# Optimization experiments

Hardware: AMD Instinct MI355X
Metric: run time of the kernel (lower is better)

## Reference

```python
import jax, jax.numpy as jnp
import numpy as np

N_ACTIONS = 4
R_DIM = 32
A_DIM = 32
FORGET = 0.05
Q_INIT = 0.0
B, T = 8192, 1024


def setup_inputs() -> dict:
    key = jax.random.key(0)
    ks = jax.random.split(key, 10)
    actions = jax.random.randint(ks[0], (B, T), 0, N_ACTIONS, dtype=jnp.int64 if jax.config.jax_enable_x64 else jnp.int32)
    rewards = jax.random.uniform(ks[1], (B, T), dtype=jnp.float32)
    s = 0.1
    w_r1 = jax.random.normal(ks[2], (R_DIM, 1 + R_DIM), dtype=jnp.float32) * s
    b_r1 = jax.random.normal(ks[3], (R_DIM,), dtype=jnp.float32) * s
    w_r2 = jax.random.normal(ks[4], (1, R_DIM), dtype=jnp.float32) * s
    b_r2 = jax.random.normal(ks[5], (1,), dtype=jnp.float32) * s
    w_a1 = jax.random.normal(ks[6], (A_DIM, N_ACTIONS + A_DIM), dtype=jnp.float32) * s
    b_a1 = jax.random.normal(ks[7], (A_DIM,), dtype=jnp.float32) * s
    w_a2 = jax.random.normal(ks[8], (N_ACTIONS, A_DIM), dtype=jnp.float32) * s
    b_a2 = jax.random.normal(ks[9], (N_ACTIONS,), dtype=jnp.float32) * s
    return {"actions": actions, "rewards": rewards,
            "w_r1": w_r1, "b_r1": b_r1, "w_r2": w_r2, "b_r2": b_r2,
            "w_a1": w_a1, "b_a1": b_a1, "w_a2": w_a2, "b_a2": b_a2}


def reference(actions, rewards, w_r1, b_r1, w_r2, b_r2, w_a1, b_a1, w_a2, b_a2):
    Bsz = actions.shape[0]
    q0 = jnp.full((Bsz, N_ACTIONS), Q_INIT, dtype=jnp.float32)
    sr0 = jnp.zeros((Bsz, R_DIM), dtype=jnp.float32)
    sa0 = jnp.zeros((Bsz, A_DIM), dtype=jnp.float32)

    def step(carry, xs):
        q, sr, sa = carry
        a_prev, r_prev = xs                        # [B] int, [B] float
        a_onehot = jax.nn.one_hot(a_prev, N_ACTIONS, dtype=jnp.float32)
        # reward module
        x_r = jnp.concatenate([r_prev[:, None], sr], axis=-1)   # [B, 1+R]
        sr_t = jnp.tanh(x_r @ w_r1.T + b_r1)                    # [B, R]
        q_new = sr_t @ w_r2.T + b_r2                            # [B, 1]
        # decay + chosen update
        q_decay = q + FORGET * (Q_INIT - q)
        q_t = q_decay * (1.0 - a_onehot) + q_new * a_onehot
        # action-history module
        x_a = jnp.concatenate([a_onehot, sa], axis=-1)          # [B, A+4]
        sa_t = jnp.tanh(x_a @ w_a1.T + b_a1)                    # [B, A]
        c_t = sa_t @ w_a2.T + b_a2                              # [B, 4]
        logits = q_t + c_t
        return (q_t, sr_t, sa_t), logits

    xs = (actions[:, :-1].T, rewards[:, :-1].T)   # time-major [T-1, B]
    _, logits_tm = jax.lax.scan(step, (q0, sr0, sa0), xs)
    return jnp.transpose(logits_tm, (1, 0, 2))    # [B, T-1, 4]
```

## Files before the change

kernel.cpp:

```cpp
#include <hip/hip_runtime.h>

#define TL 1024
#define NT 1023

typedef __bf16 bf16x8 __attribute__((ext_vector_type(8)));
typedef float  f32x4  __attribute__((ext_vector_type(4)));

__device__ __forceinline__ f32x4 mfma_bf16(bf16x8 a, bf16x8 b, f32x4 c) {
  return __builtin_amdgcn_mfma_f32_16x16x32_bf16(a, b, c, 0, 0, 0);
}

__device__ __forceinline__ unsigned pk_hi(unsigned e, unsigned o) {
  return __builtin_amdgcn_perm(o, e, 0x07060302u);
}

__device__ __forceinline__ float fast_tanh(float x) {
  float e = __builtin_amdgcn_exp2f(x * 2.8853900817779268f);
  float r = __builtin_amdgcn_rcpf(e + 1.0f);
  return fmaf(-2.0f, r, 1.0f);
}

__device__ __forceinline__ void split8(const float x[8], bf16x8& hi, bf16x8& lo) {
  unsigned h[4], l[4];
#pragma unroll
  for (int j = 0; j < 4; ++j) {
    unsigned eu = __float_as_uint(x[2 * j]);
    unsigned ou = __float_as_uint(x[2 * j + 1]);
    h[j] = pk_hi(eu, ou);
    float el = x[2 * j]     - __uint_as_float(eu & 0xFFFF0000u);
    float ol = x[2 * j + 1] - __uint_as_float(ou & 0xFFFF0000u);
    l[j] = pk_hi(__float_as_uint(el), __float_as_uint(ol));
  }
  hi = __builtin_bit_cast(bf16x8, make_uint4(h[0], h[1], h[2], h[3]));
  lo = __builtin_bit_cast(bf16x8, make_uint4(l[0], l[1], l[2], l[3]));
}

__global__ __launch_bounds__(128, 1) void memann_kernel(
    const int* __restrict__ actions, const float* __restrict__ rewards,
    const float* __restrict__ w_r1, const float* __restrict__ b_r1,
    const float* __restrict__ w_r2, const float* __restrict__ b_r2,
    const float* __restrict__ w_a1, const float* __restrict__ b_a1,
    const float* __restrict__ w_a2, const float* __restrict__ b_a2,
    float* __restrict__ out) {
  const int tid = threadIdx.x;
  const int wid = tid >> 6;
  const int l   = tid & 63;
  const int b0  = blockIdx.x * 16;
  const int m  = l & 15;
  const int ga = l >> 4;
  const int c  = l & 15;
  const int gD = l >> 4;

  __shared__ __align__(16) float tbl[2][4][64][4];
  __shared__ __align__(16) float csb[2][8][64];

  if (wid == 1) {
#pragma unroll
    for (int h = 0; h < 2; ++h)
#pragma unroll
      for (int a = 0; a < 4; ++a)
#pragma unroll
        for (int i = 0; i < 4; ++i) {
          const int row = 8 * gD + 4 * h + i;
          tbl[h][a][l][i] = b_a1[row] + w_a1[row * 36 + a];
        }
  }
  __syncthreads();

  const uint4 z4 = make_uint4(0u, 0u, 0u, 0u);
  const f32x4 zero = {0.f, 0.f, 0.f, 0.f};
  const int rowA = 8 * (m >> 2) + (m & 3);
  float wt[8];
  const int* arow = actions + (size_t)(b0 + c) * TL;

  if (wid == 0) {
    bf16x8 AWr_h[2], AWr_l[2], AQ_h, AQ_l;
#pragma unroll
    for (int h = 0; h < 2; ++h) {
#pragma unroll
      for (int i = 0; i < 8; ++i)
        wt[i] = w_r1[(rowA + 4 * h) * 33 + 1 + 8 * ga + i];
      split8(wt, AWr_h[h], AWr_l[h]);
    }
#pragma unroll
    for (int i = 0; i < 8; ++i) wt[i] = w_r2[8 * ga + i];
    split8(wt, AQ_h, AQ_l);

    float br1p[8], wr0p[8];
#pragma unroll
    for (int i = 0; i < 4; ++i) {
      br1p[i]     = b_r1[8 * gD + i];
      wr0p[i]     = w_r1[(8 * gD + i) * 33];
      br1p[4 + i] = b_r1[8 * gD + 4 + i];
      wr0p[4 + i] = w_r1[(8 * gD + 4 + i) * 33];
    }
    const float br2  = b_r2[0];
    const float ba2g = b_a2[gD];

    const float* rrow = rewards + (size_t)(b0 + c) * TL;
    float* outp = out + (size_t)(b0 + c) * NT * 4 + gD;

    int4   a_cur[2], a_nxt[2];
    float4 r_cur[2], r_nxt[2];
    a_cur[0] = *(const int4*)(arow);
    a_cur[1] = *(const int4*)(arow + 4);
    r_cur[0] = *(const float4*)(rrow);
    r_cur[1] = *(const float4*)(rrow + 4);
    a_nxt[0] = *(const int4*)(arow + 8);
    a_nxt[1] = *(const int4*)(arow + 12);
    r_nxt[0] = *(const float4*)(rrow + 8);
    r_nxt[1] = *(const float4*)(rrow + 12);

    bf16x8 Bh = __builtin_bit_cast(bf16x8, z4), Bl = Bh;
    float qv = 0.0f;
    float qreg[8];

    for (int cI = 0; cI < 128; ++cI) {
#pragma unroll
      for (int j = 0; j < 8; ++j) {
        const int4   av = a_cur[j >> 2];
        const float4 rv = r_cur[j >> 2];
        const int   a  = ((j & 3) == 0) ? av.x : ((j & 3) == 1) ? av.y
                        : ((j & 3) == 2) ? av.z : av.w;
        const float rc = ((j & 3) == 0) ? rv.x : ((j & 3) == 1) ? rv.y
                        : ((j & 3) == 2) ? rv.z : rv.w;

        f32x4 cR0, cR1;
#pragma unroll
        for (int i = 0; i < 4; ++i) {
          cR0[i] = fmaf(wr0p[i],     rc, br1p[i]);
          cR1[i] = fmaf(wr0p[4 + i], rc, br1p[4 + i]);
        }

        f32x4 dR0 = mfma_bf16(AWr_h[0], Bh, cR0);
        f32x4 dR1 = mfma_bf16(AWr_h[1], Bh, cR1);
        dR0 = mfma_bf16(AWr_h[0], Bl, dR0);
        dR1 = mfma_bf16(AWr_h[1], Bl, dR1);
        dR0 = mfma_bf16(AWr_l[0], Bh, dR0);
        dR1 = mfma_bf16(AWr_l[1], Bh, dR1);

        float xr[8];
#pragma unroll
        for (int i = 0; i < 4; ++i) {
          xr[i]     = fast_tanh(dR0[i]);
          xr[4 + i] = fast_tanh(dR1[i]);
        }
        split8(xr, Bh, Bl);

        f32x4 dq = mfma_bf16(AQ_h, Bh, zero);
        dq = mfma_bf16(AQ_h, Bl, dq);
        dq = mfma_bf16(AQ_l, Bh, dq);

        const float qn = dq[0] + br2;
        qv = (a == gD) ? qn : qv * 0.95f;
        qreg[j] = qv;
      }

      __syncthreads();

      const float* cb = &csb[cI & 1][0][0];
#pragma unroll
      for (int j = 0; j < 8; ++j) {
        const int t = 8 * cI + j;
        if (t < NT) outp[(size_t)t * 4] = (qreg[j] + cb[j * 64 + l]) + ba2g;
      }

      a_cur[0] = a_nxt[0];  a_cur[1] = a_nxt[1];
      r_cur[0] = r_nxt[0];  r_cur[1] = r_nxt[1];
      int tp = 8 * cI + 16;
      if (tp > TL - 8) tp = TL - 8;
      a_nxt[0] = *(const int4*)(arow + tp);
      a_nxt[1] = *(const int4*)(arow + tp + 4);
      r_nxt[0] = *(const float4*)(rrow + tp);
      r_nxt[1] = *(const float4*)(rrow + tp + 4);
    }
  } else {
    bf16x8 AWa_h[2], AWa_l[2], AC_h, AC_l;
#pragma unroll
    for (int h = 0; h < 2; ++h) {
#pragma unroll
      for (int i = 0; i < 8; ++i)
        wt[i] = w_a1[(rowA + 4 * h) * 36 + 4 + 8 * ga + i];
      split8(wt, AWa_h[h], AWa_l[h]);
    }
#pragma unroll
    for (int i = 0; i < 8; ++i) wt[i] = w_a2[(m & 3) * 32 + 8 * ga + i];
    split8(wt, AC_h, AC_l);

    int4 a_cur[2], a_nxt[2];
    a_cur[0] = *(const int4*)(arow);
    a_cur[1] = *(const int4*)(arow + 4);
    a_nxt[0] = *(const int4*)(arow + 8);
    a_nxt[1] = *(const int4*)(arow + 12);

    bf16x8 Bh = __builtin_bit_cast(bf16x8, z4), Bl = Bh;

    for (int cI = 0; cI < 128; ++cI) {
      float* cb = &csb[cI & 1][0][0];
#pragma unroll
      for (int j = 0; j < 8; ++j) {
        const int4 av = a_cur[j >> 2];
        const int  a  = ((j & 3) == 0) ? av.x : ((j & 3) == 1) ? av.y
                       : ((j & 3) == 2) ? av.z : av.w;

        const f32x4 pa0 = *(const f32x4*)&tbl[0][a][l][0];
        const f32x4 pa1 = *(const f32x4*)&tbl[1][a][l][0];

        f32x4 dA0 = mfma_bf16(AWa_h[0], Bh, zero);
        f32x4 dA1 = mfma_bf16(AWa_h[1], Bh, zero);
        dA0 = mfma_bf16(AWa_h[0], Bl, dA0);
        dA1 = mfma_bf16(AWa_h[1], Bl, dA1);
        dA0 = mfma_bf16(AWa_l[0], Bh, dA0);
        dA1 = mfma_bf16(AWa_l[1], Bh, dA1);

        float xa[8];
#pragma unroll
        for (int i = 0; i < 4; ++i) {
          xa[i]     = fast_tanh(dA0[i] + pa0[i]);
          xa[4 + i] = fast_tanh(dA1[i] + pa1[i]);
        }
        split8(xa, Bh, Bl);

        f32x4 dc = mfma_bf16(AC_h, Bh, zero);
        dc = mfma_bf16(AC_h, Bl, dc);
        dc = mfma_bf16(AC_l, Bh, dc);

        const float cs = (gD & 2) ? ((gD & 1) ? dc[3] : dc[2])
                                  : ((gD & 1) ? dc[1] : dc[0]);
        cb[j * 64 + l] = cs;
      }

      __syncthreads();

      a_cur[0] = a_nxt[0];  a_cur[1] = a_nxt[1];
      int tp = 8 * cI + 16;
      if (tp > TL - 8) tp = TL - 8;
      a_nxt[0] = *(const int4*)(arow + tp);
      a_nxt[1] = *(const int4*)(arow + tp + 4);
    }
  }
}


extern "C" void kernel_launch(void* const* d_in, const int* in_sizes, int n_in,
                              void* d_out, int out_size, void* d_ws,
                              size_t ws_size, hipStream_t stream) {
  const int* actions = (const int*)d_in[0];
  const float* rewards = (const float*)d_in[1];
  const float* w_r1 = (const float*)d_in[2];
  const float* b_r1 = (const float*)d_in[3];
  const float* w_r2 = (const float*)d_in[4];
  const float* b_r2 = (const float*)d_in[5];
  const float* w_a1 = (const float*)d_in[6];
  const float* b_a1 = (const float*)d_in[7];
  const float* w_a2 = (const float*)d_in[8];
  const float* b_a2 = (const float*)d_in[9];
  float* out = (float*)d_out;

  const int B = in_sizes[0] / TL;
  const int blocks = B / 16;

  hipLaunchKernelGGL(memann_kernel, dim3(blocks), dim3(128), 0, stream,
                     actions, rewards, w_r1, b_r1, w_r2, b_r2, w_a1, b_a1,
                     w_a2, b_a2, out);
}
```

Measured before the change: 678.7 us.

## Interleave two independent batch groups per wave to hide recurrence latency

Each block now handles 32 batch rows instead of 16, and each wave runs two independent recurrences interleaved in software. While one group's MFMA chain is in flight, the other group's tanh, split and head MFMAs run, with sched_barrier fences keeping that order. The aim is to hide the serial MFMA-to-tanh dependency latency of the scan. The cost is half as many blocks (256 for this batch size), more registers per wave, and a one-step skew in output indexing that has to be handled correctly.

```diff
diff --git a/kernel.cpp b/kernel.cpp
--- a/kernel.cpp
+++ b/kernel.cpp
@@ -34,6 +34,63 @@
   hi = __builtin_bit_cast(bf16x8, make_uint4(h[0], h[1], h[2], h[3]));
   lo = __builtin_bit_cast(bf16x8, make_uint4(l[0], l[1], l[2], l[3]));
 }
+
+static __device__ __forceinline__ int exti(const int4 v[2], int j) {
+  const int4 w = v[j >> 2];
+  return (j & 3) == 0 ? w.x : (j & 3) == 1 ? w.y : (j & 3) == 2 ? w.z : w.w;
+}
+static __device__ __forceinline__ float extf(const float4 v[2], int j) {
+  const float4 w = v[j >> 2];
+  return (j & 3) == 0 ? w.x : (j & 3) == 1 ? w.y : (j & 3) == 2 ? w.z : w.w;
+}
+
+__device__ __forceinline__ void rec6(const bf16x8& Ah0, const bf16x8& Ah1,
+                                     const bf16x8& Al0, const bf16x8& Al1,
+                                     const bf16x8& Bh, const bf16x8& Bl,
+                                     const f32x4& c0, const f32x4& c1,
+                                     f32x4& o0, f32x4& o1) {
+  f32x4 d0 = mfma_bf16(Ah0, Bh, c0);
+  f32x4 d1 = mfma_bf16(Ah1, Bh, c1);
+  d0 = mfma_bf16(Ah0, Bl, d0);
+  d1 = mfma_bf16(Ah1, Bl, d1);
+  d0 = mfma_bf16(Al0, Bh, d0);
+  d1 = mfma_bf16(Al1, Bh, d1);
+  o0 = d0;  o1 = d1;
+}
+
+__device__ __forceinline__ f32x4 head3(const bf16x8& Ah, const bf16x8& Al,
+                                       const bf16x8& Bh, const bf16x8& Bl) {
+  const f32x4 zf = {0.f, 0.f, 0.f, 0.f};
+  f32x4 d = mfma_bf16(Ah, Bh, zf);
+  d = mfma_bf16(Ah, Bl, d);
+  d = mfma_bf16(Al, Bh, d);
+  return d;
+}
+
+__device__ __forceinline__ void tsR(const f32x4& p0, const f32x4& p1,
+                                    bf16x8& Bh, bf16x8& Bl) {
+  float x[8];
+#pragma unroll
+  for (int i = 0; i < 4; ++i) {
+    x[i]     = fast_tanh(p0[i]);
+    x[4 + i] = fast_tanh(p1[i]);
+  }
+  split8(x, Bh, Bl);
+}
+
+__device__ __forceinline__ void tsA(const f32x4& p0, const f32x4& p1,
+                                    const f32x4& q0, const f32x4& q1,
+                                    bf16x8& Bh, bf16x8& Bl) {
+  float x[8];
+#pragma unroll
+  for (int i = 0; i < 4; ++i) {
+    x[i]     = fast_tanh(p0[i] + q0[i]);
+    x[4 + i] = fast_tanh(p1[i] + q1[i]);
+  }
+  split8(x, Bh, Bl);
+}
+
+#define SB0() __builtin_amdgcn_sched_barrier(0)
 
 __global__ __launch_bounds__(128, 1) void memann_kernel(
     const int* __restrict__ actions, const float* __restrict__ rewards,
@@ -45,14 +102,14 @@
   const int tid = threadIdx.x;
   const int wid = tid >> 6;
   const int l   = tid & 63;
-  const int b0  = blockIdx.x * 16;
+  const int b0  = blockIdx.x * 32;
   const int m  = l & 15;
   const int ga = l >> 4;
   const int c  = l & 15;
   const int gD = l >> 4;
 
   __shared__ __align__(16) float tbl[2][4][64][4];
-  __shared__ __align__(16) float csb[2][8][64];
+  __shared__ __align__(16) float csb[2][2][8][64];
 
   if (wid == 1) {
 #pragma unroll
@@ -68,23 +125,23 @@
   __syncthreads();
 
   const uint4 z4 = make_uint4(0u, 0u, 0u, 0u);
-  const f32x4 zero = {0.f, 0.f, 0.f, 0.f};
   const int rowA = 8 * (m >> 2) + (m & 3);
   float wt[8];
-  const int* arow = actions + (size_t)(b0 + c) * TL;
+
+  const int* arow0 = actions + (size_t)(b0 + c) * TL;
+  const int* arow1 = actions + (size_t)(b0 + 16 + c) * TL;
 
   if (wid == 0) {
-    bf16x8 AWr_h[2], AWr_l[2], AQ_h, AQ_l;
-#pragma unroll
-    for (int h = 0; h < 2; ++h) {
-#pragma unroll
-      for (int i = 0; i < 8; ++i)
-        wt[i] = w_r1[(rowA + 4 * h) * 33 + 1 + 8 * ga + i];
-      split8(wt, AWr_h[h], AWr_l[h]);
-    }
+    bf16x8 AWh0, AWh1, AWl0, AWl1, AQh, AQl;
+#pragma unroll
+    for (int i = 0; i < 8; ++i) wt[i] = w_r1[rowA * 33 + 1 + 8 * ga + i];
+    split8(wt, AWh0, AWl0);
+#pragma unroll
+    for (int i = 0; i < 8; ++i) wt[i] = w_r1[(rowA + 4) * 33 + 1 + 8 * ga + i];
+    split8(wt, AWh1, AWl1);
 #pragma unroll
     for (int i = 0; i < 8; ++i) wt[i] = w_r2[8 * ga + i];
-    split8(wt, AQ_h, AQ_l);
+    split8(wt, AQh, AQl);
 
     float br1p[8], wr0p[8];
 #pragma unroll
@@ -97,146 +154,161 @@
     const float br2  = b_r2[0];
     const float ba2g = b_a2[gD];
 
-    const float* rrow = rewards + (size_t)(b0 + c) * TL;
-    float* outp = out + (size_t)(b0 + c) * NT * 4 + gD;
-
-    int4   a_cur[2], a_nxt[2];
-    float4 r_cur[2], r_nxt[2];
-    a_cur[0] = *(const int4*)(arow);
-    a_cur[1] = *(const int4*)(arow + 4);
-    r_cur[0] = *(const float4*)(rrow);
-    r_cur[1] = *(const float4*)(rrow + 4);
-    a_nxt[0] = *(const int4*)(arow + 8);
-    a_nxt[1] = *(const int4*)(arow + 12);
-    r_nxt[0] = *(const float4*)(rrow + 8);
-    r_nxt[1] = *(const float4*)(rrow + 12);
-
-    bf16x8 Bh = __builtin_bit_cast(bf16x8, z4), Bl = Bh;
-    float qv = 0.0f;
-    float qreg[8];
+    const float* rrow0 = rewards + (size_t)(b0 + c) * TL;
+    const float* rrow1 = rewards + (size_t)(b0 + 16 + c) * TL;
+    float* outp0 = out + (size_t)(b0 + c) * NT * 4 + gD;
+    float* outp1 = out + (size_t)(b0 + 16 + c) * NT * 4 + gD;
+
+    int4   a0c[2], a0n[2], a1c[2], a1n[2];
+    float4 r0c[2], r0n[2], r1c[2], r1n[2];
+    a0c[0] = *(const int4*)(arow0);      a0c[1] = *(const int4*)(arow0 + 4);
+    a1c[0] = *(const int4*)(arow1);      a1c[1] = *(const int4*)(arow1 + 4);
+    r0c[0] = *(const float4*)(rrow0);    r0c[1] = *(const float4*)(rrow0 + 4);
+    r1c[0] = *(const float4*)(rrow1);    r1c[1] = *(const float4*)(rrow1 + 4);
+    a0n[0] = *(const int4*)(arow0 + 8);  a0n[1] = *(const int4*)(arow0 + 12);
+    a1n[0] = *(const int4*)(arow1 + 8);  a1n[1] = *(const int4*)(arow1 + 12);
+    r0n[0] = *(const float4*)(rrow0 + 8); r0n[1] = *(const float4*)(rrow0 + 12);
+    r1n[0] = *(const float4*)(rrow1 + 8); r1n[1] = *(const float4*)(rrow1 + 12);
+
+    bf16x8 Bh0 = __builtin_bit_cast(bf16x8, z4), Bl0 = Bh0;
+    bf16x8 Bh1 = Bh0, Bl1 = Bh0;
+    f32x4 pR00, pR01, pR10, pR11;
+    f32x4 dqp0, dqp1;
+    float qv0 = 0.f, qv1 = 0.f;
+    float qreg0[8], qreg1[8];
+    int a_last0 = 0, a_last1 = 0;
 
     for (int cI = 0; cI < 128; ++cI) {
 #pragma unroll
-      for (int j = 0; j < 8; ++j) {
-        const int4   av = a_cur[j >> 2];
-        const float4 rv = r_cur[j >> 2];
-        const int   a  = ((j & 3) == 0) ? av.x : ((j & 3) == 1) ? av.y
-                        : ((j & 3) == 2) ? av.z : av.w;
-        const float rc = ((j & 3) == 0) ? rv.x : ((j & 3) == 1) ? rv.y
-                        : ((j & 3) == 2) ? rv.z : rv.w;
-
-        f32x4 cR0, cR1;
+      for (int u = 0; u < 8; ++u) {
+        const float rc0 = extf(r0c, u);
+        const float rc1 = extf(r1c, u);
+        const int aq0 = (u == 0) ? a_last0 : exti(a0c, u - 1);
+        const int aq1 = (u == 0) ? a_last1 : exti(a1c, u - 1);
+
+        f32x4 c00, c01;
 #pragma unroll
         for (int i = 0; i < 4; ++i) {
-          cR0[i] = fmaf(wr0p[i],     rc, br1p[i]);
-          cR1[i] = fmaf(wr0p[4 + i], rc, br1p[4 + i]);
-        }
-
-        f32x4 dR0 = mfma_bf16(AWr_h[0], Bh, cR0);
-        f32x4 dR1 = mfma_bf16(AWr_h[1], Bh, cR1);
-        dR0 = mfma_bf16(AWr_h[0], Bl, dR0);
-        dR1 = mfma_bf16(AWr_h[1], Bl, dR1);
-        dR0 = mfma_bf16(AWr_l[0], Bh, dR0);
-        dR1 = mfma_bf16(AWr_l[1], Bh, dR1);
-
-        float xr[8];
+          c00[i] = fmaf(wr0p[i],     rc0, br1p[i]);
+          c01[i] = fmaf(wr0p[4 + i], rc0, br1p[4 + i]);
+        }
+        rec6(AWh0, AWh1, AWl0, AWl1, Bh0, Bl0, c00, c01, pR00, pR01);
+        if (u != 0 || cI != 0) {
+          tsR(pR10, pR11, Bh1, Bl1);
+          dqp1 = head3(AQh, AQl, Bh1, Bl1);
+          const float qn0 = dqp0[0] + br2;
+          qv0 = (aq0 == gD) ? qn0 : qv0 * 0.95f;
+          qreg0[u] = qv0;
+        }
+        SB0();
+
+        f32x4 c10, c11;
 #pragma unroll
         for (int i = 0; i < 4; ++i) {
-          xr[i]     = fast_tanh(dR0[i]);
-          xr[4 + i] = fast_tanh(dR1[i]);
-        }
-        split8(xr, Bh, Bl);
-
-        f32x4 dq = mfma_bf16(AQ_h, Bh, zero);
-        dq = mfma_bf16(AQ_h, Bl, dq);
-        dq = mfma_bf16(AQ_l, Bh, dq);
-
-        const float qn = dq[0] + br2;
-        qv = (a == gD) ? qn : qv * 0.95f;
-        qreg[j] = qv;
+          c10[i] = fmaf(wr0p[i],     rc1, br1p[i]);
+          c11[i] = fmaf(wr0p[4 + i], rc1, br1p[4 + i]);
+        }
+        rec6(AWh0, AWh1, AWl0, AWl1, Bh1, Bl1, c10, c11, pR10, pR11);
+        tsR(pR00, pR01, Bh0, Bl0);
+        dqp0 = head3(AQh, AQl, Bh0, Bl0);
+        if (u != 0 || cI != 0) {
+          const float qn1 = dqp1[0] + br2;
+          qv1 = (aq1 == gD) ? qn1 : qv1 * 0.95f;
+          qreg1[u] = qv1;
+        }
+        SB0();
       }
 
+      a_last0 = a0c[1].w;
+      a_last1 = a1c[1].w;
+
       __syncthreads();
 
-      const float* cb = &csb[cI & 1][0][0];
-#pragma unroll
-      for (int j = 0; j < 8; ++j) {
-        const int t = 8 * cI + j;
-        if (t < NT) outp[(size_t)t * 4] = (qreg[j] + cb[j * 64 + l]) + ba2g;
+      const float* cb0 = &csb[cI & 1][0][0][0];
+      const float* cb1 = &csb[cI & 1][1][0][0];
+#pragma unroll
+      for (int u = 0; u < 8; ++u) {
+        if (u != 0 || cI != 0) {
+          const int tq = 8 * cI + u - 1;
+          outp0[(size_t)tq * 4] = (qreg0[u] + cb0[u * 64 + l]) + ba2g;
+          outp1[(size_t)tq * 4] = (qreg1[u] + cb1[u * 64 + l]) + ba2g;
+        }
       }
 
-      a_cur[0] = a_nxt[0];  a_cur[1] = a_nxt[1];
-      r_cur[0] = r_nxt[0];  r_cur[1] = r_nxt[1];
+      a0c[0] = a0n[0]; a0c[1] = a0n[1]; a1c[0] = a1n[0]; a1c[1] = a1n[1];
+      r0c[0] = r0n[0]; r0c[1] = r0n[1]; r1c[0] = r1n[0]; r1c[1] = r1n[1];
       int tp = 8 * cI + 16;
       if (tp > TL - 8) tp = TL - 8;
-      a_nxt[0] = *(const int4*)(arow + tp);
-      a_nxt[1] = *(const int4*)(arow + tp + 4);
-      r_nxt[0] = *(const float4*)(rrow + tp);
-      r_nxt[1] = *(const float4*)(rrow + tp + 4);
+      a0n[0] = *(const int4*)(arow0 + tp);  a0n[1] = *(const int4*)(arow0 + tp + 4);
+      a1n[0] = *(const int4*)(arow1 + tp);  a1n[1] = *(const int4*)(arow1 + tp + 4);
+      r0n[0] = *(const float4*)(rrow0 + tp); r0n[1] = *(const float4*)(rrow0 + tp + 4);
+      r1n[0] = *(const float4*)(rrow1 + tp); r1n[1] = *(const float4*)(rrow1 + tp + 4);
     }
   } else {
-    bf16x8 AWa_h[2], AWa_l[2], AC_h, AC_l;
-#pragma unroll
-    for (int h = 0; h < 2; ++h) {
-#pragma unroll
-      for (int i = 0; i < 8; ++i)
-        wt[i] = w_a1[(rowA + 4 * h) * 36 + 4 + 8 * ga + i];
-      split8(wt, AWa_h[h], AWa_l[h]);
-    }
+    bf16x8 AWh0, AWh1, AWl0, AWl1, ACh, ACl;
+#pragma unroll
+    for (int i = 0; i < 8; ++i) wt[i] = w_a1[rowA * 36 + 4 + 8 * ga + i];
+    split8(wt, AWh0, AWl0);
+#pragma unroll
+    for (int i = 0; i < 8; ++i) wt[i] = w_a1[(rowA + 4) * 36 + 4 + 8 * ga + i];
+    split8(wt, AWh1, AWl1);
 #pragma unroll
     for (int i = 0; i < 8; ++i) wt[i] = w_a2[(m & 3) * 32 + 8 * ga + i];
-    split8(wt, AC_h, AC_l);
-
-    int4 a_cur[2], a_nxt[2];
-    a_cur[0] = *(const int4*)(arow);
-    a_cur[1] = *(const int4*)(arow + 4);
-    a_nxt[0] = *(const int4*)(arow + 8);
-    a_nxt[1] = *(const int4*)(arow + 12);
-
-    bf16x8 Bh = __builtin_bit_cast(bf16x8, z4), Bl = Bh;
+    split8(wt, ACh, ACl);
+
+    int4 a0c[2], a0n[2], a1c[2], a1n[2];
+    a0c[0] = *(const int4*)(arow0);      a0c[1] = *(const int4*)(arow0 + 4);
+    a1c[0] = *(const int4*)(arow1);      a1c[1] = *(const int4*)(arow1 + 4);
+    a0n[0] = *(const int4*)(arow0 + 8);  a0n[1] = *(const int4*)(arow0 + 12);
+    a1n[0] = *(const int4*)(arow1 + 8);  a1n[1] = *(const int4*)(arow1 + 12);
+
+    bf16x8 Bh0 = __builtin_bit_cast(bf16x8, z4), Bl0 = Bh0;
+    bf16x8 Bh1 = Bh0, Bl1 = Bh0;
+    const f32x4 zf = {0.f, 0.f, 0.f, 0.f};
+    f32x4 pA00, pA01, pA10, pA11;
+    f32x4 pa00, pa01, pa10, pa11;
+    f32x4 dcp0, dcp1;
 
     for (int cI = 0; cI < 128; ++cI) {
-      float* cb = &csb[cI & 1][0][0];
-#pragma unroll
-      for (int j = 0; j < 8; ++j) {
-        const int4 av = a_cur[j >> 2];
-        const int  a  = ((j & 3) == 0) ? av.x : ((j & 3) == 1) ? av.y
-                       : ((j & 3) == 2) ? av.z : av.w;
-
-        const f32x4 pa0 = *(const f32x4*)&tbl[0][a][l][0];
-        const f32x4 pa1 = *(const f32x4*)&tbl[1][a][l][0];
-
-        f32x4 dA0 = mfma_bf16(AWa_h[0], Bh, zero);
-        f32x4 dA1 = mfma_bf16(AWa_h[1], Bh, zero);
-        dA0 = mfma_bf16(AWa_h[0], Bl, dA0);
-        dA1 = mfma_bf16(AWa_h[1], Bl, dA1);
-        dA0 = mfma_bf16(AWa_l[0], Bh, dA0);
-        dA1 = mfma_bf16(AWa_l[1], Bh, dA1);
-
-        float xa[8];
-#pragma unroll
-        for (int i = 0; i < 4; ++i) {
-          xa[i]     = fast_tanh(dA0[i] + pa0[i]);
-          xa[4 + i] = fast_tanh(dA1[i] + pa1[i]);
-        }
-        split8(xa, Bh, Bl);
-
-        f32x4 dc = mfma_bf16(AC_h, Bh, zero);
-        dc = mfma_bf16(AC_h, Bl, dc);
-        dc = mfma_bf16(AC_l, Bh, dc);
-
-        const float cs = (gD & 2) ? ((gD & 1) ? dc[3] : dc[2])
-                                  : ((gD & 1) ? dc[1] : dc[0]);
-        cb[j * 64 + l] = cs;
+      float* cw0 = &csb[cI & 1][0][0][0];
+      float* cw1 = &csb[cI & 1][1][0][0];
+#pragma unroll
+      for (int u = 0; u < 8; ++u) {
+        const int a0 = exti(a0c, u);
+        const int a1 = exti(a1c, u);
+
+        pa00 = *(const f32x4*)&tbl[0][a0][l][0];
+        pa01 = *(const f32x4*)&tbl[1][a0][l][0];
+        rec6(AWh0, AWh1, AWl0, AWl1, Bh0, Bl0, zf, zf, pA00, pA01);
+        if (u != 0 || cI != 0) {
+          tsA(pA10, pA11, pa10, pa11, Bh1, Bl1);
+          dcp1 = head3(ACh, ACl, Bh1, Bl1);
+          const float cs0 = (gD & 2) ? ((gD & 1) ? dcp0[3] : dcp0[2])
+                                     : ((gD & 1) ? dcp0[1] : dcp0[0]);
+          cw0[u * 64 + l] = cs0;
+        }
+        SB0();
+
+        pa10 = *(const f32x4*)&tbl[0][a1][l][0];
+        pa11 = *(const f32x4*)&tbl[1][a1][l][0];
+        rec6(AWh0, AWh1, AWl0, AWl1, Bh1, Bl1, zf, zf, pA10, pA11);
+        tsA(pA00, pA01, pa00, pa01, Bh0, Bl0);
+        dcp0 = head3(ACh, ACl, Bh0, Bl0);
+        if (u != 0 || cI != 0) {
+          const float cs1 = (gD & 2) ? ((gD & 1) ? dcp1[3] : dcp1[2])
+                                     : ((gD & 1) ? dcp1[1] : dcp1[0]);
+          cw1[u * 64 + l] = cs1;
+        }
+        SB0();
       }
 
       __syncthreads();
 
-      a_cur[0] = a_nxt[0];  a_cur[1] = a_nxt[1];
+      a0c[0] = a0n[0]; a0c[1] = a0n[1]; a1c[0] = a1n[0]; a1c[1] = a1n[1];
       int tp = 8 * cI + 16;
       if (tp > TL - 8) tp = TL - 8;
-      a_nxt[0] = *(const int4*)(arow + tp);
-      a_nxt[1] = *(const int4*)(arow + tp + 4);
+      a0n[0] = *(const int4*)(arow0 + tp);  a0n[1] = *(const int4*)(arow0 + tp + 4);
+      a1n[0] = *(const int4*)(arow1 + tp);  a1n[1] = *(const int4*)(arow1 + tp + 4);
     }
   }
 }
@@ -258,7 +330,7 @@
   float* out = (float*)d_out;
 
   const int B = in_sizes[0] / TL;
-  const int blocks = B / 16;
+  const int blocks = B / 32;
 
   hipLaunchKernelGGL(memann_kernel, dim3(blocks), dim3(128), 0, stream,
                      actions, rewards, w_r1, b_r1, w_r2, b_r2, w_a1, b_a1,
```

Result: slower. 745.2 us (+9.8%).
